# Kernel optimization log

Measured on AMD Instinct MI355X. Metric: run time of the kernel, lower is better.

Reference implementation:

```python
import jax, jax.numpy as jnp
import numpy as np

N_DEG = 5
RANK = 4
SCALE = 4
IMW = IMH = 512
S = IMW * IMH
BATCH = 64
C_CH = 1


def setup_inputs() -> dict:
    key = jax.random.key(0)
    k1, k2, k3, k4 = jax.random.split(key, 4)
    x = jax.random.normal(k1, (BATCH, C_CH, IMW // SCALE, IMH // SCALE), dtype=jnp.float32)
    # CP-decomposed polynomial (CCP) factors; small init keeps degree-5 products stable
    A = jax.random.normal(k2, (N_DEG, RANK, S), dtype=jnp.float32) * 0.01
    C = jax.random.normal(k3, (S, RANK), dtype=jnp.float32) * 0.01
    b = jax.random.normal(k4, (S,), dtype=jnp.float32) * 0.01
    return {"x": x, "A": A, "C": C, "b": b}


def reference(x, A, C, b):
    bsize, c, w, h = x.shape
    # bilinear upsample, align_corners=False (half-pixel, matches torch default)
    up = jax.image.resize(x, (bsize, c, w * SCALE, h * SCALE), method="bilinear")
    flat = up.reshape(bsize, c, S)
    v = flat[:, c - 1, :]  # [B, S] -- original applies PolyLayer only to channel c-1
    # CCP polynomial network: z1 = A1 v; z_n = (A_n v) * z_{n-1} + z_{n-1}
    za = jnp.einsum("nrs,bs->bnr", A, v)  # [B, N, rank]
    z = za[:, 0]
    for n in range(1, N_DEG):
        z = za[:, n] * z + z
    out_v = jnp.einsum("br,sr->bs", z, C) + b  # [B, S]
    flat = flat.at[:, c - 1, :].set(out_v)
    return flat.reshape(bsize, c, w * SCALE, h * SCALE)
```

## Files before the change

kernel.cpp:

```cpp
#include <hip/hip_runtime.h>

#define S_TOTAL (512 * 512)
#define BATCH 64
#define NPR 16

typedef float vfloat4 __attribute__((ext_vector_type(4)));

__device__ __forceinline__ float swz_x1(float v) {
    return __int_as_float(__builtin_amdgcn_ds_swizzle(__float_as_int(v), 0x041F));
}
__device__ __forceinline__ float swz_x2(float v) {
    return __int_as_float(__builtin_amdgcn_ds_swizzle(__float_as_int(v), 0x081F));
}
__device__ __forceinline__ float swz_x4(float v) {
    return __int_as_float(__builtin_amdgcn_ds_swizzle(__float_as_int(v), 0x101F));
}
__device__ __forceinline__ float swz_x8(float v) {
    return __int_as_float(__builtin_amdgcn_ds_swizzle(__float_as_int(v), 0x201F));
}

__global__ __launch_bounds__(256) void fused_za_kernel(
    const float* __restrict__ x,
    const float* __restrict__ A,
    float* __restrict__ partial)
{
    __shared__ float b1loc[36][128];
    __shared__ float b2loc[1024];

    const int t   = threadIdx.x;
    const int blk = blockIdx.x;
    const int rest = blk >> 3;
    const int tcp  = (rest / 40) * 8 + (blk & 7);
    const int r40  = rest % 40;
    const int nr   = r40 >> 1;
    const int bh   = r40 & 1;
    const int y0   = 32 * tcp - 2;

    const float* An = A + (size_t)nr * S_TOTAL;

    for (int i = t; i < 36 * 128; i += 256) {
        const int rl = i >> 7;
        const int j  = i & 127;
        const int y  = y0 + rl;
        float s = 0.0f;
        if (y >= 0 && y < 512) {
            const float* Ay = An + (size_t)y * 512;
            const int base = 4 * j;
            const vfloat4 m0 = *(const vfloat4*)(Ay + max(base - 4, 0));
            const vfloat4 m1 = *(const vfloat4*)(Ay + base);
            const vfloat4 m2 = *(const vfloat4*)(Ay + min(base + 4, 508));
            float e0 = m0.z, e1 = m0.w, e6 = m2.x, e7 = m2.y;
            if (j == 0)   { e0 = 0.0f; e1 = 0.0f; }
            if (j == 127) { e6 = 0.0f; e7 = 0.0f; }
            s = 0.125f * e0 + 0.375f * e1
              + 0.625f * m1.x + 0.875f * m1.y
              + 0.875f * m1.z + 0.625f * m1.w
              + 0.375f * e6 + 0.125f * e7;
            if (j == 0)   s += 0.375f * Ay[0]   + 0.125f * Ay[1];
            if (j == 127) s += 0.125f * Ay[510] + 0.375f * Ay[511];
        }
        b1loc[rl][j] = s;
    }
    __syncthreads();

    const float w[8] = {0.125f, 0.375f, 0.625f, 0.875f,
                        0.875f, 0.625f, 0.375f, 0.125f};
#pragma unroll
    for (int i = t; i < 1024; i += 256) {
        const int tyl = i >> 7;
        const int j   = i & 127;
        const int ty  = tcp * 8 + tyl;
        float s = 0.0f;
#pragma unroll
        for (int p = 0; p < 8; ++p)
            s = fmaf(w[p], b1loc[4 * tyl + p][j], s);
        if (ty == 0)   s += 0.375f * b1loc[2][j]  + 0.125f * b1loc[3][j];
        if (ty == 127) s += 0.125f * b1loc[32][j] + 0.375f * b1loc[33][j];
        b2loc[i] = s;
    }
    __syncthreads();

    const int wv   = t >> 6;
    const int lane = t & 63;
    const int b0   = bh * 32 + wv * 8;
    const size_t xbase = (size_t)tcp * 1024 + 4 * lane;

    const vfloat4 bq0 = *(const vfloat4*)&b2loc[4 * lane];
    const vfloat4 bq1 = *(const vfloat4*)&b2loc[4 * lane + 256];
    const vfloat4 bq2 = *(const vfloat4*)&b2loc[4 * lane + 512];
    const vfloat4 bq3 = *(const vfloat4*)&b2loc[4 * lane + 768];

    float acc[8];
#pragma unroll
    for (int bi = 0; bi < 8; ++bi) {
        const float* xb = x + (size_t)(b0 + bi) * 16384 + xbase;
        const vfloat4 x0 = *(const vfloat4*)(xb);
        const vfloat4 x1 = *(const vfloat4*)(xb + 256);
        const vfloat4 x2 = *(const vfloat4*)(xb + 512);
        const vfloat4 x3 = *(const vfloat4*)(xb + 768);
        float a = 0.0f;
        a = fmaf(bq0.x, x0.x, fmaf(bq0.y, x0.y, fmaf(bq0.z, x0.z, fmaf(bq0.w, x0.w, a))));
        a = fmaf(bq1.x, x1.x, fmaf(bq1.y, x1.y, fmaf(bq1.z, x1.z, fmaf(bq1.w, x1.w, a))));
        a = fmaf(bq2.x, x2.x, fmaf(bq2.y, x2.y, fmaf(bq2.z, x2.z, fmaf(bq2.w, x2.w, a))));
        a = fmaf(bq3.x, x3.x, fmaf(bq3.y, x3.y, fmaf(bq3.z, x3.z, fmaf(bq3.w, x3.w, a))));
        acc[bi] = a;
    }

    const int lane1 = lane & 1, lane2 = lane & 2, lane4 = lane & 4;
    float s1[4];
#pragma unroll
    for (int v = 0; v < 4; ++v) {
        const float u = acc[v], h = acc[v + 4];
        s1[v] = (lane1 ? h : u) + swz_x1(lane1 ? u : h);
    }
    float s2[2];
#pragma unroll
    for (int v = 0; v < 2; ++v) {
        const float u = s1[v], h = s1[v + 2];
        s2[v] = (lane2 ? h : u) + swz_x2(lane2 ? u : h);
    }
    float s3;
    {
        const float u = s2[0], h = s2[1];
        s3 = (lane4 ? h : u) + swz_x4(lane4 ? u : h);
    }
    s3 += swz_x8(s3);
    s3 += __shfl_xor(s3, 16, 64);
    s3 += __shfl_xor(s3, 32, 64);

    if (lane < 8) {
        const int m = ((lane & 1) << 2) | (lane & 2) | ((lane & 4) >> 2);
        partial[(size_t)tcp * 1280 + (b0 + m) * 20 + nr] = s3;
    }
}

__global__ __launch_bounds__(256) void out_kernel(
    const float* __restrict__ C,
    const float* __restrict__ bias,
    const float* __restrict__ partial,
    float* __restrict__ out)
{
    __shared__ float za_sh[1280];
    __shared__ float zs[256];
    const int t = threadIdx.x;

    const int sb = blockIdx.x >> 1;
    const int bh = blockIdx.x & 1;
    const int s0 = (sb * 256 + t) * 4;
    const vfloat4 c0 = *(const vfloat4*)(C + (size_t)s0 * 4);
    const vfloat4 c1 = *(const vfloat4*)(C + (size_t)s0 * 4 + 4);
    const vfloat4 c2 = *(const vfloat4*)(C + (size_t)s0 * 4 + 8);
    const vfloat4 c3 = *(const vfloat4*)(C + (size_t)s0 * 4 + 12);
    const vfloat4 bv = *(const vfloat4*)(bias + s0);

#pragma unroll
    for (int qq = 0; qq < 5; ++qq) {
        const int c = qq * 256 + t;
        float a0 = 0, a1 = 0, a2 = 0, a3 = 0;
#pragma unroll
        for (int r = 0; r < NPR; r += 4) {
            a0 += partial[(size_t)(r + 0) * 1280 + c];
            a1 += partial[(size_t)(r + 1) * 1280 + c];
            a2 += partial[(size_t)(r + 2) * 1280 + c];
            a3 += partial[(size_t)(r + 3) * 1280 + c];
        }
        za_sh[c] = (a0 + a1) + (a2 + a3);
    }
    __syncthreads();
    if (t < 64) {
#pragma unroll
        for (int r = 0; r < 4; ++r) {
            float zv = za_sh[t * 20 + r];
#pragma unroll
            for (int n = 1; n < 5; ++n)
                zv *= (1.0f + za_sh[t * 20 + n * 4 + r]);
            zs[t * 4 + r] = zv;
        }
    }
    __syncthreads();

#pragma unroll 8
    for (int bb = bh * 32; bb < bh * 32 + 32; ++bb) {
        const float z0 = zs[bb * 4 + 0], z1 = zs[bb * 4 + 1];
        const float z2 = zs[bb * 4 + 2], z3 = zs[bb * 4 + 3];
        vfloat4 o;
        o.x = fmaf(z0, c0.x, fmaf(z1, c0.y, fmaf(z2, c0.z, fmaf(z3, c0.w, bv.x))));
        o.y = fmaf(z0, c1.x, fmaf(z1, c1.y, fmaf(z2, c1.z, fmaf(z3, c1.w, bv.y))));
        o.z = fmaf(z0, c2.x, fmaf(z1, c2.y, fmaf(z2, c2.z, fmaf(z3, c2.w, bv.z))));
        o.w = fmaf(z0, c3.x, fmaf(z1, c3.y, fmaf(z2, c3.z, fmaf(z3, c3.w, bv.w))));
        __builtin_nontemporal_store(o, (vfloat4*)(out + (size_t)bb * S_TOTAL + s0));
    }
}

extern "C" void kernel_launch(void* const* d_in, const int* in_sizes, int n_in,
                              void* d_out, int out_size, void* d_ws, size_t ws_size,
                              hipStream_t stream)
{
    const float* x    = (const float*)d_in[0];
    const float* A    = (const float*)d_in[1];
    const float* C    = (const float*)d_in[2];
    const float* bias = (const float*)d_in[3];
    float* out = (float*)d_out;

    float* partial = (float*)d_ws;

    fused_za_kernel<<<640, 256, 0, stream>>>(x, A, partial);
    out_kernel<<<512, 256, 0, stream>>>(C, bias, partial, out);
}
```

Before: 34.40 us.

## Halve rows per za block and give each wave sixteen batches

Each za block now covers 16 image rows (4 low-res rows) for all 64 batches, instead of 32 rows for half the batches. The A-side downsample halo work per block drops, and the A reads are no longer duplicated across two batch-half blocks. In exchange, each wave reduces 16 batch accumulators through an extra swizzle stage, and out_kernel must sum 32 partial rows instead of 16. The grid stays at 640 blocks, but the halo overhead is now relatively larger, since 20 rows are loaded to produce 16.

```diff
diff --git a/kernel.cpp b/kernel.cpp
--- a/kernel.cpp
+++ b/kernel.cpp
@@ -2,7 +2,7 @@
 
 #define S_TOTAL (512 * 512)
 #define BATCH 64
-#define NPR 16
+#define NPR 32
 
 typedef float vfloat4 __attribute__((ext_vector_type(4)));
 
@@ -24,21 +24,19 @@
     const float* __restrict__ A,
     float* __restrict__ partial)
 {
-    __shared__ float b1loc[36][128];
-    __shared__ float b2loc[1024];
+    __shared__ float b1loc[20][128];
+    __shared__ float b2loc[512];
 
     const int t   = threadIdx.x;
     const int blk = blockIdx.x;
     const int rest = blk >> 3;
-    const int tcp  = (rest / 40) * 8 + (blk & 7);
-    const int r40  = rest % 40;
-    const int nr   = r40 >> 1;
-    const int bh   = r40 & 1;
-    const int y0   = 32 * tcp - 2;
+    const int tc   = (rest / 20) * 8 + (blk & 7);
+    const int nr   = rest % 20;
+    const int y0   = 16 * tc - 2;
 
     const float* An = A + (size_t)nr * S_TOTAL;
 
-    for (int i = t; i < 36 * 128; i += 256) {
+    for (int i = t; i < 20 * 128; i += 256) {
         const int rl = i >> 7;
         const int j  = i & 127;
         const int y  = y0 + rl;
@@ -66,71 +64,71 @@
     const float w[8] = {0.125f, 0.375f, 0.625f, 0.875f,
                         0.875f, 0.625f, 0.375f, 0.125f};
 #pragma unroll
-    for (int i = t; i < 1024; i += 256) {
+    for (int i = t; i < 512; i += 256) {
         const int tyl = i >> 7;
         const int j   = i & 127;
-        const int ty  = tcp * 8 + tyl;
+        const int ty  = tc * 4 + tyl;
         float s = 0.0f;
 #pragma unroll
         for (int p = 0; p < 8; ++p)
             s = fmaf(w[p], b1loc[4 * tyl + p][j], s);
         if (ty == 0)   s += 0.375f * b1loc[2][j]  + 0.125f * b1loc[3][j];
-        if (ty == 127) s += 0.125f * b1loc[32][j] + 0.375f * b1loc[33][j];
+        if (ty == 127) s += 0.125f * b1loc[16][j] + 0.375f * b1loc[17][j];
         b2loc[i] = s;
     }
     __syncthreads();
 
     const int wv   = t >> 6;
     const int lane = t & 63;
-    const int b0   = bh * 32 + wv * 8;
-    const size_t xbase = (size_t)tcp * 1024 + 4 * lane;
+    const int b0   = wv * 16;
+    const size_t xbase = (size_t)tc * 512 + 4 * lane;
 
     const vfloat4 bq0 = *(const vfloat4*)&b2loc[4 * lane];
     const vfloat4 bq1 = *(const vfloat4*)&b2loc[4 * lane + 256];
-    const vfloat4 bq2 = *(const vfloat4*)&b2loc[4 * lane + 512];
-    const vfloat4 bq3 = *(const vfloat4*)&b2loc[4 * lane + 768];
-
-    float acc[8];
-#pragma unroll
-    for (int bi = 0; bi < 8; ++bi) {
+
+    float acc[16];
+#pragma unroll
+    for (int bi = 0; bi < 16; ++bi) {
         const float* xb = x + (size_t)(b0 + bi) * 16384 + xbase;
         const vfloat4 x0 = *(const vfloat4*)(xb);
         const vfloat4 x1 = *(const vfloat4*)(xb + 256);
-        const vfloat4 x2 = *(const vfloat4*)(xb + 512);
-        const vfloat4 x3 = *(const vfloat4*)(xb + 768);
         float a = 0.0f;
         a = fmaf(bq0.x, x0.x, fmaf(bq0.y, x0.y, fmaf(bq0.z, x0.z, fmaf(bq0.w, x0.w, a))));
         a = fmaf(bq1.x, x1.x, fmaf(bq1.y, x1.y, fmaf(bq1.z, x1.z, fmaf(bq1.w, x1.w, a))));
-        a = fmaf(bq2.x, x2.x, fmaf(bq2.y, x2.y, fmaf(bq2.z, x2.z, fmaf(bq2.w, x2.w, a))));
-        a = fmaf(bq3.x, x3.x, fmaf(bq3.y, x3.y, fmaf(bq3.z, x3.z, fmaf(bq3.w, x3.w, a))));
         acc[bi] = a;
     }
 
-    const int lane1 = lane & 1, lane2 = lane & 2, lane4 = lane & 4;
-    float s1[4];
+    const int lane1 = lane & 1, lane2 = lane & 2, lane4 = lane & 4, lane8 = lane & 8;
+    float s1[8];
+#pragma unroll
+    for (int v = 0; v < 8; ++v) {
+        const float u = acc[v], h = acc[v + 8];
+        s1[v] = (lane1 ? h : u) + swz_x1(lane1 ? u : h);
+    }
+    float s2[4];
 #pragma unroll
     for (int v = 0; v < 4; ++v) {
-        const float u = acc[v], h = acc[v + 4];
-        s1[v] = (lane1 ? h : u) + swz_x1(lane1 ? u : h);
-    }
-    float s2[2];
+        const float u = s1[v], h = s1[v + 4];
+        s2[v] = (lane2 ? h : u) + swz_x2(lane2 ? u : h);
+    }
+    float s3[2];
 #pragma unroll
     for (int v = 0; v < 2; ++v) {
-        const float u = s1[v], h = s1[v + 2];
-        s2[v] = (lane2 ? h : u) + swz_x2(lane2 ? u : h);
-    }
-    float s3;
+        const float u = s2[v], h = s2[v + 2];
+        s3[v] = (lane4 ? h : u) + swz_x4(lane4 ? u : h);
+    }
+    float s4;
     {
-        const float u = s2[0], h = s2[1];
-        s3 = (lane4 ? h : u) + swz_x4(lane4 ? u : h);
-    }
-    s3 += swz_x8(s3);
-    s3 += __shfl_xor(s3, 16, 64);
-    s3 += __shfl_xor(s3, 32, 64);
-
-    if (lane < 8) {
-        const int m = ((lane & 1) << 2) | (lane & 2) | ((lane & 4) >> 2);
-        partial[(size_t)tcp * 1280 + (b0 + m) * 20 + nr] = s3;
+        const float u = s3[0], h = s3[1];
+        s4 = (lane8 ? h : u) + swz_x8(lane8 ? u : h);
+    }
+    s4 += __shfl_xor(s4, 16, 64);
+    s4 += __shfl_xor(s4, 32, 64);
+
+    if (lane < 16) {
+        const int m = ((lane & 1) << 3) | ((lane & 2) << 1) |
+                      ((lane & 4) >> 1) | ((lane & 8) >> 3);
+        partial[(size_t)tc * 1280 + (b0 + m) * 20 + nr] = s4;
     }
 }
 
```

New measurement: 47.90 us. +39.2%, slower.
